# Optimization experiments

Hardware: AMD Instinct MI355X
Metric: run time of the kernel (lower is better)

Reference implementation:

```python
import jax, jax.numpy as jnp
import numpy as np

NUM_CLASSES = 80
IMAGE_W, IMAGE_H = 608.0, 608.0
XY_SCALE = 1.05
BOXES_PER_CELL = 3
# anchors selected by anchor_ids=[0,1,2] from the canonical YOLOv3 COCO anchor_dims
ANCHOR_WH = np.array([[10.0, 13.0], [16.0, 30.0], [33.0, 23.0]], dtype=np.float32)


def setup_inputs() -> dict:
    key = jax.random.key(0)
    x = jax.random.normal(key, (32, BOXES_PER_CELL * (NUM_CLASSES + 5), 76, 76), dtype=jnp.float32)
    return {"x": x}


def reference(x):
    B, C, H, W = x.shape
    num_attrs = NUM_CLASSES + 5
    # [B, C, H, W] -> [B, H, W, boxes_per_cell, num_attrs]
    x = jnp.transpose(x, (0, 2, 3, 1)).reshape(B, H, W, BOXES_PER_CELL, num_attrs)

    xy = jax.nn.sigmoid(x[..., :2]) * XY_SCALE - 0.5 * (XY_SCALE - 1.0)
    wh = x[..., 2:4]
    confidence = jax.nn.sigmoid(x[..., 4:5])
    classprob = jax.nn.sigmoid(x[..., 5:])

    # global xy: add per-cell grid offsets, normalize by grid size
    gx, gy = jnp.meshgrid(jnp.arange(W, dtype=x.dtype), jnp.arange(H, dtype=x.dtype))  # [H, W]
    offset = jnp.stack((gx, gy), -1)[None, :, :, None, :]  # [1, H, W, 1, 2] (x, y)
    grid_size = jnp.array([W, H], dtype=x.dtype)
    image_xy = (xy + offset) / grid_size

    # scale wh by anchor priors, normalize to [0, 1] by image size
    anchor_wh = jnp.asarray(ANCHOR_WH, dtype=x.dtype)  # [boxes_per_cell, 2]
    image_size = jnp.array([IMAGE_W, IMAGE_H], dtype=x.dtype)
    image_wh = jnp.exp(wh) * anchor_wh / image_size

    # center/size -> corner coordinates
    half_wh = image_wh * 0.5
    boxes = jnp.concatenate((image_xy - half_wh, image_xy + half_wh), -1)

    output = jnp.concatenate((boxes, confidence, classprob), -1)
    return output.reshape(B, H * W * BOXES_PER_CELL, num_attrs)
```

## Files before the change

### kernel.cpp

```cpp
#include <hip/hip_runtime.h>


#define NUM_ATTRS 85
#define HWSZ 5776
#define TILE 64
#define NTILES 91
#define LDS_STRIDE (TILE + 1)

__device__ __forceinline__ float fsigmoid(float x) {
    return 1.0f / (1.0f + __expf(-x));
}

__global__ __launch_bounds__(256) void detect_kernel(const float* __restrict__ in,
                                                     float* __restrict__ out) {
    __shared__ float tile[NUM_ATTRS * LDS_STRIDE];

    const int tix = blockIdx.x;
    const int box = blockIdx.y;
    const int b   = blockIdx.z;
    const int tid = threadIdx.x;

    const int s0   = tix * TILE;
    const int npos = min(TILE, HWSZ - s0);
    const int n4   = npos >> 2;

    const float awk[3] = {10.0f / 1216.0f, 16.0f / 1216.0f, 33.0f / 1216.0f};
    const float ahk[3] = {13.0f / 1216.0f, 30.0f / 1216.0f, 23.0f / 1216.0f};
    const float aw = awk[box];
    const float ah = ahk[box];

    const float* __restrict__ src = in + ((size_t)b * 255 + (size_t)box * 85) * HWSZ;

#pragma unroll
    for (int it = 0; it < 6; ++it) {
        const int i = tid + it * 256;
        if (i < NUM_ATTRS * (TILE >> 2)) {
            const int attr = i >> 4;
            const int c4   = i & 15;
            if (c4 < n4) {
                const int pos = s0 + c4 * 4;
                const float4 v = *reinterpret_cast<const float4*>(src + (size_t)attr * HWSZ + pos);
                float r[4] = {v.x, v.y, v.z, v.w};
#pragma unroll
                for (int j = 0; j < 4; ++j) {
                    const int p = pos + j;
                    const float x = r[j];
                    float o;
                    if (attr >= 4) {
                        o = fsigmoid(x);
                    } else if (attr == 0) {
                        const float w = (float)(p % 76);
                        o = (fsigmoid(x) * 1.05f - 0.025f + w) * (1.0f / 76.0f);
                    } else if (attr == 1) {
                        const float h = (float)(p / 76);
                        o = (fsigmoid(x) * 1.05f - 0.025f + h) * (1.0f / 76.0f);
                    } else if (attr == 2) {
                        o = __expf(x) * aw;
                    } else {
                        o = __expf(x) * ah;
                    }
                    tile[attr * LDS_STRIDE + c4 * 4 + j] = o;
                }
            }
        }
    }
    __syncthreads();

    float* __restrict__ dst = out + (size_t)b * (HWSZ * 3 * 85)
                                  + (size_t)s0 * 255 + (size_t)box * 85;
    const int total = npos * NUM_ATTRS;
    for (int i = tid; i < total; i += 256) {
        const int p    = i / 85;
        const int attr = i - p * 85;
        float v;
        if (attr < 4) {
            const int base = attr & 1;
            const float c  = tile[base * LDS_STRIDE + p];
            const float hf = tile[(base + 2) * LDS_STRIDE + p];
            v = (attr < 2) ? (c - hf) : (c + hf);
        } else {
            v = tile[attr * LDS_STRIDE + p];
        }
        dst[(size_t)p * 255 + attr] = v;
    }
}

extern "C" void kernel_launch(void* const* d_in, const int* in_sizes, int n_in,
                              void* d_out, int out_size, void* d_ws, size_t ws_size,
                              hipStream_t stream) {
    const float* x = (const float*)d_in[0];
    float* out = (float*)d_out;
    dim3 grid(NTILES, 3, 32);
    detect_kernel<<<grid, 256, 0, stream>>>(x, out);
}
```

Before: 339.8 us.

## Tile all 255 channels per block for contiguous float4 output stores

```diff
diff --git a/kernel.cpp b/kernel.cpp
--- a/kernel.cpp
+++ b/kernel.cpp
@@ -1,11 +1,11 @@
 #include <hip/hip_runtime.h>
 
 
-#define NUM_ATTRS 85
 #define HWSZ 5776
-#define TILE 64
-#define NTILES 91
-#define LDS_STRIDE (TILE + 1)
+#define TILE 16
+#define NTILES 361
+#define NCH 255
+#define LDS_DW (TILE * NCH)
 
 __device__ __forceinline__ float fsigmoid(float x) {
     return 1.0f / (1.0f + __expf(-x));
@@ -13,75 +13,68 @@
 
 __global__ __launch_bounds__(256) void detect_kernel(const float* __restrict__ in,
                                                      float* __restrict__ out) {
-    __shared__ float tile[NUM_ATTRS * LDS_STRIDE];
+    __shared__ float tile[LDS_DW];
 
-    const int tix = blockIdx.x;
-    const int box = blockIdx.y;
-    const int b   = blockIdx.z;
+    const int x   = blockIdx.x;
+    const int xcd = x & 7;
+    const int idx = x >> 3;
+    const int tix = (xcd == 0 ? 0 : 46 + (xcd - 1) * 45) + idx;
+
+    const int b   = blockIdx.y;
     const int tid = threadIdx.x;
+    const int s0  = tix * TILE;
 
-    const int s0   = tix * TILE;
-    const int npos = min(TILE, HWSZ - s0);
-    const int n4   = npos >> 2;
-
-    const float awk[3] = {10.0f / 1216.0f, 16.0f / 1216.0f, 33.0f / 1216.0f};
-    const float ahk[3] = {13.0f / 1216.0f, 30.0f / 1216.0f, 23.0f / 1216.0f};
-    const float aw = awk[box];
-    const float ah = ahk[box];
-
-    const float* __restrict__ src = in + ((size_t)b * 255 + (size_t)box * 85) * HWSZ;
+    const float* __restrict__ src = in + (size_t)b * NCH * HWSZ;
 
 #pragma unroll
-    for (int it = 0; it < 6; ++it) {
+    for (int it = 0; it < 4; ++it) {
         const int i = tid + it * 256;
-        if (i < NUM_ATTRS * (TILE >> 2)) {
-            const int attr = i >> 4;
-            const int c4   = i & 15;
-            if (c4 < n4) {
-                const int pos = s0 + c4 * 4;
-                const float4 v = *reinterpret_cast<const float4*>(src + (size_t)attr * HWSZ + pos);
-                float r[4] = {v.x, v.y, v.z, v.w};
+        if (i < NCH * (TILE / 4)) {
+            const int c   = i >> 2;
+            const int c4  = i & 3;
+            const int box = (c >= 170) ? 2 : (c >= 85 ? 1 : 0);
+            const int sub = c - box * 85;
+            const int pos = s0 + c4 * 4;
+
+            if (sub >= 4) {
+                const float4 v = *reinterpret_cast<const float4*>(src + (size_t)c * HWSZ + pos);
+                const float r[4] = {v.x, v.y, v.z, v.w};
+#pragma unroll
+                for (int j = 0; j < 4; ++j)
+                    tile[(c4 * 4 + j) * NCH + c] = fsigmoid(r[j]);
+            } else if (sub < 2) {
+                float aw;
+                if (sub == 0)
+                    aw = (box == 0) ? 10.0f / 1216.0f : ((box == 1) ? 16.0f / 1216.0f : 33.0f / 1216.0f);
+                else
+                    aw = (box == 0) ? 13.0f / 1216.0f : ((box == 1) ? 30.0f / 1216.0f : 23.0f / 1216.0f);
+                const float4 vx = *reinterpret_cast<const float4*>(src + (size_t)c * HWSZ + pos);
+                const float4 vw = *reinterpret_cast<const float4*>(src + (size_t)(c + 2) * HWSZ + pos);
+                const float rx[4] = {vx.x, vx.y, vx.z, vx.w};
+                const float rw[4] = {vw.x, vw.y, vw.z, vw.w};
 #pragma unroll
                 for (int j = 0; j < 4; ++j) {
-                    const int p = pos + j;
-                    const float x = r[j];
-                    float o;
-                    if (attr >= 4) {
-                        o = fsigmoid(x);
-                    } else if (attr == 0) {
-                        const float w = (float)(p % 76);
-                        o = (fsigmoid(x) * 1.05f - 0.025f + w) * (1.0f / 76.0f);
-                    } else if (attr == 1) {
-                        const float h = (float)(p / 76);
-                        o = (fsigmoid(x) * 1.05f - 0.025f + h) * (1.0f / 76.0f);
-                    } else if (attr == 2) {
-                        o = __expf(x) * aw;
-                    } else {
-                        o = __expf(x) * ah;
-                    }
-                    tile[attr * LDS_STRIDE + c4 * 4 + j] = o;
+                    const int p  = pos + j;
+                    const int ph = p / 76;
+                    const float coord = (sub == 0) ? (float)(p - ph * 76) : (float)ph;
+                    const float ctr  = (fsigmoid(rx[j]) * 1.05f - 0.025f + coord) * (1.0f / 76.0f);
+                    const float half = __expf(rw[j]) * aw;
+                    tile[(c4 * 4 + j) * NCH + c]     = ctr - half;
+                    tile[(c4 * 4 + j) * NCH + c + 2] = ctr + half;
                 }
             }
         }
     }
     __syncthreads();
 
-    float* __restrict__ dst = out + (size_t)b * (HWSZ * 3 * 85)
-                                  + (size_t)s0 * 255 + (size_t)box * 85;
-    const int total = npos * NUM_ATTRS;
-    for (int i = tid; i < total; i += 256) {
-        const int p    = i / 85;
-        const int attr = i - p * 85;
-        float v;
-        if (attr < 4) {
-            const int base = attr & 1;
-            const float c  = tile[base * LDS_STRIDE + p];
-            const float hf = tile[(base + 2) * LDS_STRIDE + p];
-            v = (attr < 2) ? (c - hf) : (c + hf);
-        } else {
-            v = tile[attr * LDS_STRIDE + p];
+    float* __restrict__ dst = out + (size_t)b * ((size_t)HWSZ * NCH) + (size_t)s0 * NCH;
+#pragma unroll
+    for (int it = 0; it < 4; ++it) {
+        const int i = tid + it * 256;
+        if (i < LDS_DW / 4) {
+            const float4 v = *reinterpret_cast<const float4*>(tile + 4 * i);
+            *reinterpret_cast<float4*>(dst + 4 * i) = v;
         }
-        dst[(size_t)p * 255 + attr] = v;
     }
 }
 
@@ -90,6 +83,6 @@
                               hipStream_t stream) {
     const float* x = (const float*)d_in[0];
     float* out = (float*)d_out;
-    dim3 grid(NTILES, 3, 32);
+    dim3 grid(NTILES, 32);
     detect_kernel<<<grid, 256, 0, stream>>>(x, out);
 }
```

After: 308.2 us. -9.3%, faster.
